# Performance work log

Measured on AMD Instinct MI355X. Metric: run time of the kernel, lower is better.

## Reference

```python
import jax, jax.numpy as jnp
from jax import lax
import numpy as np

N = 4096      # nnodes
D = 64        # embed_dim
R = 128       # nodes per region
G = N // R    # 32 regions (contiguous blocks)
BIG = 1e9     # 'no edge' cost (scipy MST treats zero-similarity entries as absent edges)


def setup_inputs() -> dict:
    key = jax.random.key(0)
    emb = jax.random.normal(key, (N, D), dtype=jnp.float32) * 0.05  # nn.Embedding weight (xavier-like scale)
    region_id = jnp.arange(N) // R
    inter_mask = (region_id[:, None] != region_id[None, :]).astype(jnp.float32)  # block off-diagonal buffer
    return {"emb_weight": emb, "inter_mask": inter_mask, "inter_budget": 1024}


def _prim_forest_mask(W):
    """Prim's algorithm on dense cost matrix W [R,R] (BIG = missing edge).
    Returns symmetric 0/1 minimum-spanning-FOREST edge mask, matching
    scipy.sparse.csgraph.minimum_spanning_tree on the same graph (weights distinct)."""
    r = W.shape[0]

    def step(carry, _):
        in_tree, key_, parent, mask = carry
        km = jnp.where(in_tree, BIG, key_)
        u = jnp.argmin(km)                          # cheapest node to attach
        valid = (km[u] < BIG * 0.5).astype(W.dtype)  # BIG key => start new component, no edge
        p = parent[u]
        mask = mask.at[u, p].add(valid)
        mask = mask.at[p, u].add(valid)
        in_tree = in_tree.at[u].set(True)
        wu = W[u]
        improve = (~in_tree) & (wu < key_)
        key_ = jnp.where(improve, wu, key_)
        parent = jnp.where(improve, u, parent)
        return (in_tree, key_, parent, mask), None

    in_tree0 = jnp.zeros(r, dtype=bool).at[0].set(True)
    key0 = W[0]
    parent0 = jnp.zeros(r, dtype=jnp.int32)
    mask0 = jnp.zeros_like(W)
    (_, _, _, mask), _ = lax.scan(step, (in_tree0, key0, parent0, mask0), None, length=r - 1)
    return (mask > 0).astype(W.dtype)


def reference(emb_weight, inter_mask, inter_budget):
    # adj_dense = relu(tanh(E E^T))  [N,N]
    adj = jax.nn.relu(jnp.tanh(emb_weight @ emb_weight.T))
    adj_ng = lax.stop_gradient(adj)  # torch: MST input is .detach(); top-k indices carry no grad

    # ---- intra: per-region MST (max spanning forest of similarity == min SF of -sim) ----
    blocks = adj_ng.reshape(G, R, G, R)[jnp.arange(G), :, jnp.arange(G), :]  # [G,R,R] diagonal blocks
    eye = jnp.eye(R, dtype=bool)
    W = jnp.where((blocks > 0) & ~eye, -blocks, BIG)  # zero similarity => no edge (scipy semantics)
    intra_blocks = jax.vmap(_prim_forest_mask)(W)     # [G,R,R]
    idx = jnp.arange(N).reshape(G, R)
    intra = jnp.zeros((N, N), adj.dtype).at[idx[:, :, None], idx[:, None, :]].set(intra_blocks)
    intra = intra * (1.0 - jnp.eye(N, dtype=adj.dtype))  # fill_diagonal_(0)

    # ---- inter: global top-k over upper-triangular masked similarities ----
    flat = jnp.triu(adj_ng * inter_mask, k=1).reshape(-1)  # [N*N]
    k = int(inter_budget)  # == min(budget, nnz(inter_mask)//2); budget is smaller by construction
    _, top_idx = lax.top_k(flat, k)
    inter_sel = jnp.zeros(N * N, adj.dtype).at[top_idx].set(1.0).reshape(N, N)
    inter_sel = inter_sel + inter_sel.T

    final_mask = ((intra + inter_sel) > 0).astype(adj.dtype)
    return adj * final_mask
```

## Files before the change

### kernel.cpp

```cpp
#include <hip/hip_runtime.h>

#define NN 4096
#define DD 64
#define RR 128
#define GG 32
constexpr float BIGF = 1e9f;
constexpr unsigned BIGH = 0xCE6E6B28u;
constexpr unsigned FLOOR_KEY = 0x3D000000u;
constexpr int FLOORB = 0x3D0;
constexpr int NBINS  = 64;

constexpr int WS_FH   = 0;
constexpr int WS_ECNT = 2051;
constexpr int WS_CCNT = 2052;
constexpr int WS_MIJ  = 2112;
constexpr int WS_MV   = WS_MIJ + 4096;
constexpr int WS_EI   = WS_MV + 4096;
constexpr int WS_EJ   = WS_EI + 8192;
constexpr int WS_EV   = WS_EJ + 8192;
constexpr int WS_CK   = WS_EV + 8192;
constexpr int WS_CI   = WS_CK + 8192;
constexpr int EDGE_CAP = 8192;
constexpr int CAND_CAP = 8192;

__global__ void init_kernel(unsigned* ws) {
  for (int b = threadIdx.x; b < 2112; b += 1024) ws[b] = 0;
}

__device__ __forceinline__ void pair_decode(int p, int& gi, int& gj) {
  gi = 0;
  int rem = p;
  while (rem >= GG - 1 - gi) { rem -= GG - 1 - gi; ++gi; }
  gj = gi + 1 + rem;
}

__device__ __forceinline__ void scan_bins(const unsigned* __restrict__ ws, unsigned k,
                                          unsigned* shm ,
                                          unsigned& tlo, unsigned& thi, unsigned& rem) {
  const int t = threadIdx.x;
  if (t < NBINS) shm[t] = ws[WS_FH + FLOORB + t];
  __syncthreads();
  if (t == 0) {
    unsigned cum = 0;
    int fb = FLOORB;
    unsigned r = 0;
    for (int b = NBINS - 1; b >= 0; --b) {
      unsigned c = shm[b];
      if (cum + c >= k) { fb = FLOORB + b; r = k - cum; break; }
      cum += c;
    }
    shm[64] = ((unsigned)fb) << 20;
    shm[65] = ((unsigned)(fb + 1)) << 20;
    shm[66] = r;
  }
  __syncthreads();
  tlo = shm[64];
  thi = shm[65];
  rem = shm[66];
}

__global__ __launch_bounds__(256) void gemm_adj_kernel(const float* __restrict__ E,
                                                       float* __restrict__ adj,
                                                       unsigned* __restrict__ ws) {
  const int ti = blockIdx.y, tj = blockIdx.x;
  const bool rdiag = (ti >> 1) == (tj >> 1);
  if (tj < ti && !rdiag) return;
  const bool cross = (tj >> 1) > (ti >> 1);

  __shared__ float4 As4[64 * 16];
  __shared__ float4 Bs4[64 * 16];
  __shared__ unsigned h[NBINS];
  const float4* E4 = (const float4*)E;
  const int bi = ti * 64, bj = tj * 64;
  const int tid = threadIdx.x;

  if (tid < NBINS) h[tid] = 0;

#pragma unroll
  for (int it = 0; it < 4; ++it) {
    int row = (tid >> 4) + it * 16;
    int g = tid & 15;
    int sw = g ^ ((row >> 2) & 7);
    As4[row * 16 + sw] = E4[(bi + row) * 16 + g];
    Bs4[row * 16 + sw] = E4[(bj + row) * 16 + g];
  }
  __syncthreads();

  const int i0 = (tid >> 4) * 4;
  const int j0 = (tid & 15) * 4;
  const int sa = (i0 >> 2) & 7;
  const int sb = (j0 >> 2) & 7;
  float acc[4][4] = {};
#pragma unroll 2
  for (int k4 = 0; k4 < 16; ++k4) {
    float4 av[4], bv[4];
#pragma unroll
    for (int r = 0; r < 4; ++r) av[r] = As4[(i0 + r) * 16 + (k4 ^ sa)];
#pragma unroll
    for (int c = 0; c < 4; ++c) bv[c] = Bs4[(j0 + c) * 16 + (k4 ^ sb)];
#pragma unroll
    for (int r = 0; r < 4; ++r)
#pragma unroll
      for (int c = 0; c < 4; ++c) {
        acc[r][c] += av[r].x * bv[c].x;
        acc[r][c] += av[r].y * bv[c].y;
        acc[r][c] += av[r].z * bv[c].z;
        acc[r][c] += av[r].w * bv[c].w;
      }
  }
#pragma unroll
  for (int r = 0; r < 4; ++r) {
    float4 o;
    float* p = &o.x;
#pragma unroll
    for (int c = 0; c < 4; ++c) {
      float t = tanhf(acc[r][c]);
      p[c] = t > 0.f ? t : 0.f;
    }
    *(float4*)(adj + (size_t)(bi + i0 + r) * NN + bj + j0) = o;
    if (cross) {
#pragma unroll
      for (int c = 0; c < 4; ++c) {
        unsigned key = __float_as_uint(p[c]);
        if (key >= FLOOR_KEY) atomicAdd(&h[(key >> 20) - FLOORB], 1u);
      }
    }
  }
  if (cross) {
    __syncthreads();
    if (tid < NBINS) {
      unsigned c = h[tid];
      if (c) atomicAdd(&ws[WS_FH + FLOORB + tid], c);
    }
  }
}

template <int CTRL>
__device__ __forceinline__ void dpp_min(unsigned& kh, unsigned& kl) {
  unsigned oh = (unsigned)__builtin_amdgcn_update_dpp(0, (int)kh, CTRL, 0xF, 0xF, false);
  unsigned ol = (unsigned)__builtin_amdgcn_update_dpp(0, (int)kl, CTRL, 0xF, 0xF, false);
  unsigned long long o = ((unsigned long long)oh << 32) | ol;
  unsigned long long c = ((unsigned long long)kh << 32) | kl;
  if (o < c) { kh = oh; kl = ol; }
}
__device__ __forceinline__ void shfl_min(unsigned& kh, unsigned& kl, int m) {
  unsigned oh = (unsigned)__shfl_xor((int)kh, m);
  unsigned ol = (unsigned)__shfl_xor((int)kl, m);
  unsigned long long o = ((unsigned long long)oh << 32) | ol;
  unsigned long long c = ((unsigned long long)kh << 32) | kl;
  if (o < c) { kh = oh; kl = ol; }
}
__device__ __forceinline__ unsigned xfneg(float a) {
  return ~__float_as_uint(a) & 0x7FFFFFFFu;
}

__global__ __launch_bounds__(64) void mst_kernel(const float* __restrict__ adj, unsigned* ws) {
  __shared__ float W[RR * RR];
  __shared__ unsigned emij[RR];
  __shared__ float emv[RR];
  const int g = blockIdx.x, l = threadIdx.x, base = g * RR;
  float4* W4 = (float4*)W;
  const float4* A4 = (const float4*)adj;

#pragma unroll
  for (int n = 0; n < 64; ++n) {
    int f = l + 64 * n;
    W4[f] = A4[(size_t)(base + (f >> 5)) * (NN / 4) + (base >> 2) + (f & 31)];
  }
  emij[l] = 0xFFFFFFFFu;
  emij[l + 64] = 0xFFFFFFFFu;
  __syncthreads();

  const int n0 = l, n1 = l + 64;
  float a0 = W[n0], a1 = W[n1];
  unsigned key0 = (n0 != 0 && a0 > 0.f) ? xfneg(a0) : BIGH;
  unsigned key1 = (a1 > 0.f) ? xfneg(a1) : BIGH;
  bool in0 = (l == 0), in1 = false;
  int par0 = 0, par1 = 0;

  for (int it = 0; it < RR - 1; ++it) {
    unsigned kA = in0 ? BIGH : key0;
    unsigned kB = in1 ? BIGH : key1;
    unsigned kh, kl;
    if (kB < kA) { kh = kB; kl = (unsigned)n1; }
    else         { kh = kA; kl = (unsigned)n0; }
    dpp_min<0xB1>(kh, kl);
    dpp_min<0x4E>(kh, kl);
    dpp_min<0x141>(kh, kl);
    dpp_min<0x140>(kh, kl);
    shfl_min(kh, kl, 16);
    shfl_min(kh, kl, 32);
    const int u = (int)kl;

    if (l == (u & 63)) {
      unsigned pij = 0xFFFFFFFFu;
      float pv = 0.f;
      if ((int)kh >= 0) {
        int par = (u >> 6) ? par1 : par0;
        pij = ((unsigned)(base + u) << 12) | (unsigned)(base + par);
        pv = __uint_as_float(~kh & 0x7FFFFFFFu);
      }
      emij[it] = pij;
      emv[it] = pv;
    }
    in0 = in0 || (u == n0);
    in1 = in1 || (u == n1);
    float w0v = W[u * RR + n0];
    float w1v = W[u * RR + n1];
    unsigned w0 = (w0v > 0.f && n0 != u) ? xfneg(w0v) : BIGH;
    unsigned w1 = (w1v > 0.f && n1 != u) ? xfneg(w1v) : BIGH;
    if (!in0 && w0 < key0) { key0 = w0; par0 = u; }
    if (!in1 && w1 < key1) { key1 = w1; par1 = u; }
  }
  __syncthreads();
  ws[WS_MIJ + base + l] = emij[l];
  ws[WS_MIJ + base + 64 + l] = emij[64 + l];
  ((float*)(ws + WS_MV))[base + l] = emv[l];
  ((float*)(ws + WS_MV))[base + 64 + l] = emv[64 + l];
}

__global__ __launch_bounds__(256) void collect_kernel(const float* __restrict__ adj,
                                                      unsigned* ws, const int* budget) {
  __shared__ unsigned shm[67];
  unsigned tlo, thi, rem;
  scan_bins(ws, (unsigned)budget[0], shm, tlo, thi, rem);
  (void)rem;
  int gi, gj;
  pair_decode(blockIdx.x, gi, gj);
  const float4* a4 = (const float4*)adj;
  for (int e = threadIdx.x; e < RR * 32; e += 256) {
    int r = e >> 5, c4 = e & 31;
    float4 v = a4[(size_t)(gi * RR + r) * (NN / 4) + gj * 32 + c4];
    float comp[4] = {v.x, v.y, v.z, v.w};
#pragma unroll
    for (int c = 0; c < 4; ++c) {
      float x = comp[c];
      if (!(x > 0.f)) continue;
      unsigned key = __float_as_uint(x);
      if (key < tlo) continue;
      int i = gi * RR + r, j = gj * RR + c4 * 4 + c;
      if (key >= thi) {
        unsigned slot = atomicAdd(ws + WS_ECNT, 1u);
        if (slot < EDGE_CAP) {
          ((int*)(ws + WS_EI))[slot] = i;
          ((int*)(ws + WS_EJ))[slot] = j;
          ((float*)(ws + WS_EV))[slot] = x;
        }
      } else {
        unsigned s2 = atomicAdd(ws + WS_CCNT, 1u);
        if (s2 < CAND_CAP) {
          ws[WS_CK + s2] = key;
          ws[WS_CI + s2] = (unsigned)((i << 12) | j);
        }
      }
    }
  }
}

__global__ __launch_bounds__(1024) void topk_kernel(unsigned* ws, const int* budget) {
  __shared__ unsigned long long s[CAND_CAP];
  __shared__ unsigned shm[67];
  unsigned tlo, thi, rem;
  scan_bins(ws, (unsigned)budget[0], shm, tlo, thi, rem);
  (void)tlo; (void)thi;
  const int t = threadIdx.x;
  unsigned n = ws[WS_CCNT];
  if (n > CAND_CAP) n = CAND_CAP;
  unsigned m = 2;
  while (m < n) m <<= 1;
  for (int i = t; i < (int)m; i += 1024) {
    unsigned long long v = 0ull;
    if (i < (int)n)
      v = ((unsigned long long)ws[WS_CK + i] << 32) |
          (unsigned long long)(0x00FFFFFFu - ws[WS_CI + i]);
    s[i] = v;
  }
  for (unsigned size = 2; size <= m; size <<= 1)
    for (unsigned stride = size >> 1; stride; stride >>= 1) {
      __syncthreads();
      for (unsigned i = t; i < m / 2; i += 1024) {
        unsigned lo = ((i & ~(stride - 1)) << 1) | (i & (stride - 1));
        unsigned hi = lo | stride;
        bool up = ((lo & size) == 0);
        unsigned long long a = s[lo], b = s[hi];
        if ((a > b) == up) { s[lo] = b; s[hi] = a; }
      }
    }
  __syncthreads();
  for (unsigned p = t; p < rem; p += 1024) {
    unsigned long long v = s[m - 1 - p];
    if (v == 0ull) continue;
    unsigned key = (unsigned)(v >> 32);
    unsigned idx = 0x00FFFFFFu - (unsigned)(v & 0xFFFFFFFFull);
    unsigned slot = atomicAdd(ws + WS_ECNT, 1u);
    if (slot < EDGE_CAP) {
      ((int*)(ws + WS_EI))[slot] = (int)(idx >> 12);
      ((int*)(ws + WS_EJ))[slot] = (int)(idx & 4095u);
      ((float*)(ws + WS_EV))[slot] = __uint_as_float(key);
    }
  }
}

__global__ void scatter_kernel(const unsigned* __restrict__ ws, float* __restrict__ out) {
  unsigned cnt = ws[WS_ECNT];
  if (cnt > EDGE_CAP) cnt = EDGE_CAP;
  const int tot = 4096 + (int)cnt;
  for (int e = blockIdx.x * blockDim.x + threadIdx.x; e < tot;
       e += gridDim.x * blockDim.x) {
    int i, j;
    float v;
    if (e < 4096) {
      unsigned pij = ws[WS_MIJ + e];
      if (pij == 0xFFFFFFFFu) continue;
      i = (int)(pij >> 12);
      j = (int)(pij & 4095u);
      v = ((const float*)(ws + WS_MV))[e];
    } else {
      int q = e - 4096;
      i = ((const int*)(ws + WS_EI))[q];
      j = ((const int*)(ws + WS_EJ))[q];
      v = ((const float*)(ws + WS_EV))[q];
    }
    out[(size_t)i * NN + j] = v;
    out[(size_t)j * NN + i] = v;
  }
}

extern "C" void kernel_launch(void* const* d_in, const int* in_sizes, int n_in,
                              void* d_out, int out_size, void* d_ws, size_t ws_size,
                              hipStream_t stream) {
  const float* E      = (const float*)d_in[0];
  const int*   budget = (const int*)d_in[2];
  float*    adj = (float*)d_out;
  unsigned* ws  = (unsigned*)d_ws;

  init_kernel<<<1, 1024, 0, stream>>>(ws);
  gemm_adj_kernel<<<dim3(NN / 64, NN / 64), 256, 0, stream>>>(E, adj, ws);
  mst_kernel<<<GG, 64, 0, stream>>>(adj, ws);
  collect_kernel<<<GG * (GG - 1) / 2, 256, 0, stream>>>(adj, ws, budget);
  topk_kernel<<<1, 1024, 0, stream>>>(ws, budget);
  hipMemsetAsync(d_out, 0, (size_t)NN * NN * sizeof(float), stream);
  scatter_kernel<<<64, 256, 0, stream>>>(ws, adj);
}
```

Measured before the change: 257.7 us.

## Fuse output zeroing with scatter and use DPP row broadcasts in Prim argmin

The separate memset and scatter launches are replaced by one kernel. Each of its 256 blocks zeroes a 16-row stripe of the output and then writes only the edges whose row falls in that stripe, which removes a launch and the ordering gap between zeroing and scattering. Each block rescans the whole edge list, so that small list is read redundantly. In the MST loop, the xor shuffles are replaced by DPP row_bcast steps followed by readlane of lane 63, and the parent index is fetched with readlane, so a uniform lane 0 writes the edge. This cuts cross-lane latency on the serial Prim chain.

After: 256.7 us. Within noise of the previous version (-0.4%).

```diff
diff --git a/kernel.cpp b/kernel.cpp
--- a/kernel.cpp
+++ b/kernel.cpp
@@ -137,15 +137,8 @@
 
 template <int CTRL>
 __device__ __forceinline__ void dpp_min(unsigned& kh, unsigned& kl) {
-  unsigned oh = (unsigned)__builtin_amdgcn_update_dpp(0, (int)kh, CTRL, 0xF, 0xF, false);
-  unsigned ol = (unsigned)__builtin_amdgcn_update_dpp(0, (int)kl, CTRL, 0xF, 0xF, false);
-  unsigned long long o = ((unsigned long long)oh << 32) | ol;
-  unsigned long long c = ((unsigned long long)kh << 32) | kl;
-  if (o < c) { kh = oh; kl = ol; }
-}
-__device__ __forceinline__ void shfl_min(unsigned& kh, unsigned& kl, int m) {
-  unsigned oh = (unsigned)__shfl_xor((int)kh, m);
-  unsigned ol = (unsigned)__shfl_xor((int)kl, m);
+  unsigned oh = (unsigned)__builtin_amdgcn_update_dpp((int)kh, (int)kh, CTRL, 0xF, 0xF, false);
+  unsigned ol = (unsigned)__builtin_amdgcn_update_dpp((int)kl, (int)kl, CTRL, 0xF, 0xF, false);
   unsigned long long o = ((unsigned long long)oh << 32) | ol;
   unsigned long long c = ((unsigned long long)kh << 32) | kl;
   if (o < c) { kh = oh; kl = ol; }
@@ -188,17 +181,20 @@
     dpp_min<0x4E>(kh, kl);
     dpp_min<0x141>(kh, kl);
     dpp_min<0x140>(kh, kl);
-    shfl_min(kh, kl, 16);
-    shfl_min(kh, kl, 32);
-    const int u = (int)kl;
-
-    if (l == (u & 63)) {
+    dpp_min<0x142>(kh, kl);
+    dpp_min<0x143>(kh, kl);
+    const unsigned mh = (unsigned)__builtin_amdgcn_readlane((int)kh, 63);
+    const int u = __builtin_amdgcn_readlane((int)kl, 63);
+
+    const int p0 = __builtin_amdgcn_readlane(par0, u & 63);
+    const int p1 = __builtin_amdgcn_readlane(par1, u & 63);
+    const int par = (u >> 6) ? p1 : p0;
+    if (l == 0) {
       unsigned pij = 0xFFFFFFFFu;
       float pv = 0.f;
-      if ((int)kh >= 0) {
-        int par = (u >> 6) ? par1 : par0;
+      if ((int)mh >= 0) {
         pij = ((unsigned)(base + u) << 12) | (unsigned)(base + par);
-        pv = __uint_as_float(~kh & 0x7FFFFFFFu);
+        pv = __uint_as_float(~mh & 0x7FFFFFFFu);
       }
       emij[it] = pij;
       emv[it] = pv;
@@ -301,12 +297,18 @@
   }
 }
 
-__global__ void scatter_kernel(const unsigned* __restrict__ ws, float* __restrict__ out) {
+__global__ __launch_bounds__(256) void zero_scatter_kernel(const unsigned* __restrict__ ws,
+                                                           float* __restrict__ out) {
+  const int bid = blockIdx.x;
+  const int r0 = bid * 16;
+  float4* out4 = (float4*)(out + (size_t)r0 * NN);
+  const float4 z = make_float4(0.f, 0.f, 0.f, 0.f);
+  for (int e = threadIdx.x; e < 16 * (NN / 4); e += 256) out4[e] = z;
+  __syncthreads();
   unsigned cnt = ws[WS_ECNT];
   if (cnt > EDGE_CAP) cnt = EDGE_CAP;
   const int tot = 4096 + (int)cnt;
-  for (int e = blockIdx.x * blockDim.x + threadIdx.x; e < tot;
-       e += gridDim.x * blockDim.x) {
+  for (int e = threadIdx.x; e < tot; e += 256) {
     int i, j;
     float v;
     if (e < 4096) {
@@ -321,8 +323,8 @@
       j = ((const int*)(ws + WS_EJ))[q];
       v = ((const float*)(ws + WS_EV))[q];
     }
-    out[(size_t)i * NN + j] = v;
-    out[(size_t)j * NN + i] = v;
+    if ((i >> 4) == bid) out[(size_t)i * NN + j] = v;
+    if ((j >> 4) == bid) out[(size_t)j * NN + i] = v;
   }
 }
 
@@ -339,6 +341,5 @@
   mst_kernel<<<GG, 64, 0, stream>>>(adj, ws);
   collect_kernel<<<GG * (GG - 1) / 2, 256, 0, stream>>>(adj, ws, budget);
   topk_kernel<<<1, 1024, 0, stream>>>(ws, budget);
-  hipMemsetAsync(d_out, 0, (size_t)NN * NN * sizeof(float), stream);
-  scatter_kernel<<<64, 256, 0, stream>>>(ws, adj);
-}
+  zero_scatter_kernel<<<256, 256, 0, stream>>>(ws, adj);
+}
```
